# Kernel tuning notes

Hardware: AMD Instinct MI355X
Metric: run time of the kernel (lower is better)

## Reference

```python
import jax, jax.numpy as jnp
import numpy as np

HIDDEN = 1024
BATCH = 32
SRC_LEN = 2048
NEG_BIG = -1e10


def setup_inputs() -> dict:
    key = jax.random.key(0)
    k1, k2, k3, k4, k5, k6 = jax.random.split(key, 6)
    s = 1.0 / np.sqrt(2 * HIDDEN)
    return {
        "decoder_hidden": jax.random.normal(k1, (BATCH, HIDDEN), dtype=jnp.float32),
        "encoder_outputs": jax.random.normal(k2, (BATCH, SRC_LEN, HIDDEN), dtype=jnp.float32),
        "mask": jax.random.randint(k3, (BATCH, SRC_LEN), 0, 2, dtype=jnp.int32),
        # attn: Linear(2H -> H). Store as (2H, H) so x @ W matches torch x @ W.T
        "attn_W": jax.random.uniform(k4, (2 * HIDDEN, HIDDEN), jnp.float32, -s, s),
        "attn_b": jax.random.uniform(k5, (HIDDEN,), jnp.float32, -s, s),
        # v: Linear(H -> 1, bias=False), stored as (H,)
        "v_w": jax.random.uniform(k6, (HIDDEN,), jnp.float32, -1.0 / np.sqrt(HIDDEN), 1.0 / np.sqrt(HIDDEN)),
    }


def reference(decoder_hidden, encoder_outputs, mask, attn_W, attn_b, v_w):
    # Split the concat-linear: [dec, enc] @ W == dec @ W_dec + enc @ W_enc (same math, no big concat)
    W_dec, W_enc = attn_W[:HIDDEN], attn_W[HIDDEN:]
    dec_proj = decoder_hidden @ W_dec + attn_b            # (B, H)
    enc_proj = jnp.einsum("bsh,hk->bsk", encoder_outputs, W_enc)  # (B, S, H)
    energy = jnp.tanh(dec_proj[:, None, :] + enc_proj)    # (B, S, H)
    attention = jnp.einsum("bsh,h->bs", energy, v_w)      # (B, S)
    attention = jnp.where(mask == 0, NEG_BIG, attention)
    attention_weights = jax.nn.softmax(attention, axis=1)  # (B, S)
    context = jnp.einsum("bs,bsh->bh", attention_weights, encoder_outputs)  # (B, H)
    return attention_weights, context
```

## Files before the change

### kernel.cpp

```cpp
#include <hip/hip_runtime.h>
#include <hip/hip_bf16.h>
#include <math.h>

#define HIDDEN 1024
#define BATCH 32
#define SRC_LEN 2048
#define NROWS (BATCH * SRC_LEN)
#define NEG_BIG -10000000000.0f

typedef __attribute__((ext_vector_type(8))) short bf16x8;
typedef __attribute__((ext_vector_type(4))) float f32x4;
typedef __attribute__((ext_vector_type(4))) unsigned uint32x4;

static __device__ __forceinline__ unsigned short f2bf(float f) {
  unsigned u = __float_as_uint(f);
  u = u + 0x7fffu + ((u >> 16) & 1u);
  return (unsigned short)(u >> 16);
}
static __device__ __forceinline__ unsigned pack2(float a, float b) {
  return (unsigned)f2bf(a) | ((unsigned)f2bf(b) << 16);
}

__global__ __launch_bounds__(256) void k_wt(
    const float* __restrict__ W, unsigned short* __restrict__ WT) {
  __shared__ float ts[64][65];
  const int hy = blockIdx.y * 64, nx = blockIdx.x * 64;
  const int tid = threadIdx.x;
#pragma unroll
  for (int i = 0; i < 16; ++i) {
    int idx = tid + i * 256, r = idx >> 6, c = idx & 63;
    ts[r][c] = W[(HIDDEN + hy + r) * HIDDEN + nx + c];
  }
  __syncthreads();
#pragma unroll
  for (int i = 0; i < 16; ++i) {
    int idx = tid + i * 256, rn = idx >> 6, ch = idx & 63;
    WT[(nx + rn) * HIDDEN + hy + ch] = f2bf(ts[ch][rn]);
  }
}

__global__ __launch_bounds__(256) void k_dec_part(
    const float* __restrict__ dh, const float* __restrict__ W,
    float* __restrict__ decpart) {
  const int kl = threadIdx.x & 63;
  const int bq = threadIdx.x >> 6;
  const int k = blockIdx.x * 64 + kl;
  const int h0 = blockIdx.y * 64;
  __shared__ float dh_s[64][33];
#pragma unroll
  for (int i = 0; i < 8; ++i) {
    int idx = threadIdx.x + i * 256;
    int b = idx >> 6, hh = idx & 63;
    dh_s[hh][b] = dh[b * HIDDEN + h0 + hh];
  }
  __syncthreads();
  float acc[8] = {0.f, 0.f, 0.f, 0.f, 0.f, 0.f, 0.f, 0.f};
#pragma unroll
  for (int hh = 0; hh < 64; ++hh) {
    float w = W[(h0 + hh) * HIDDEN + k];
#pragma unroll
    for (int bb = 0; bb < 8; ++bb) acc[bb] += dh_s[hh][bq * 8 + bb] * w;
  }
#pragma unroll
  for (int bb = 0; bb < 8; ++bb)
    decpart[blockIdx.y * (BATCH * HIDDEN) + (bq * 8 + bb) * HIDDEN + k] = acc[bb];
}

__global__ __launch_bounds__(256) void k_dec_reduce(
    const float* __restrict__ decpart, const float* __restrict__ bias,
    float* __restrict__ out) {
  int e = blockIdx.x * 256 + threadIdx.x;
  float s = bias[e & (HIDDEN - 1)];
#pragma unroll
  for (int hc = 0; hc < 16; ++hc) s += decpart[hc * (BATCH * HIDDEN) + e];
  out[e] = s;
}

#define BM 128
#define BN 256
#define BK 64
#define NT (HIDDEN / BK)

__global__ __launch_bounds__(512, 2) void k_energy_mfma(
    const float* __restrict__ enc, const unsigned short* __restrict__ WT,
    const float* __restrict__ dec_proj, const float* __restrict__ v_w,
    float* __restrict__ part) {
  __shared__ unsigned short As[2][BM * BK];
  __shared__ unsigned short Bs[2][BN * BK];
  __shared__ float red[4][BM];

  const int tid = threadIdx.x;
  const int lane = tid & 63;
  const int wid = tid >> 6;
  const int wm = wid >> 2;
  const int wn = wid & 3;
  const int l16 = lane & 15;
  const int kg = lane >> 4;

  const int bid = blockIdx.x;
  const int l = (bid & 7) * 256 + (bid >> 3);
  const int n0 = (l & 3) * BN;
  const int row0 = (l >> 2) * BM;
  const int b = row0 >> 11;

  f32x4 acc[4][4];
#pragma unroll
  for (int m = 0; m < 4; ++m)
#pragma unroll
    for (int n = 0; n < 4; ++n) acc[m][n] = (f32x4){0.f, 0.f, 0.f, 0.f};

  const float4* enc4 = (const float4*)enc;
  const uint32x4* WT4 = (const uint32x4*)WT;

  float4 pa[4];
  uint32x4 pb[4];

#define LOADAB(t)                                                         \
  do {                                                                    \
    int h0 = (t) * BK;                                                    \
    _Pragma("unroll") for (int i = 0; i < 4; ++i) {                       \
      int chunk = tid + i * 512;                                          \
      int r = chunk >> 4, c4 = chunk & 15;                                \
      pa[i] = enc4[(size_t)(row0 + r) * 256 + (h0 >> 2) + c4];            \
    }                                                                     \
    _Pragma("unroll") for (int i = 0; i < 4; ++i) {                       \
      int chunk = tid + i * 512;                                          \
      int nr = chunk >> 3, c16 = chunk & 7;                               \
      pb[i] = WT4[(size_t)(n0 + nr) * 128 + (h0 >> 3) + c16];             \
    }                                                                     \
  } while (0)

#define STOREAB(bufi)                                                     \
  do {                                                                    \
    _Pragma("unroll") for (int i = 0; i < 4; ++i) {                       \
      int chunk = tid + i * 512;                                          \
      int r = chunk >> 4, c4 = chunk & 15;                                \
      unsigned off = r * 128 + ((c4 * 8) ^ ((r & 7) << 4));               \
      uint2 u;                                                            \
      u.x = pack2(pa[i].x, pa[i].y);                                      \
      u.y = pack2(pa[i].z, pa[i].w);                                      \
      *(uint2*)((char*)As[bufi] + off) = u;                               \
    }                                                                     \
    _Pragma("unroll") for (int i = 0; i < 4; ++i) {                       \
      int chunk = tid + i * 512;                                          \
      int nr = chunk >> 3, c16 = chunk & 7;                               \
      unsigned off = nr * 128 + ((c16 * 16) ^ ((nr & 7) << 4));           \
      *(uint32x4*)((char*)Bs[bufi] + off) = pb[i];                        \
    }                                                                     \
  } while (0)

  LOADAB(0);
  STOREAB(0);
  __syncthreads();

  for (int t = 0; t < NT; ++t) {
    const int cur = t & 1;
    if (t + 1 < NT) LOADAB(t + 1);

    __builtin_amdgcn_s_setprio(1);
#pragma unroll
    for (int ks = 0; ks < 2; ++ks) {
      bf16x8 af[4], bv[4];
#pragma unroll
      for (int m = 0; m < 4; ++m) {
        int r = wm * 64 + m * 16 + l16;
        unsigned off = r * 128 + ((ks * 64 + kg * 16) ^ ((r & 7) << 4));
        af[m] = *(const bf16x8*)((const char*)As[cur] + off);
      }
#pragma unroll
      for (int n = 0; n < 4; ++n) {
        int c = wn * 64 + n * 16 + l16;
        unsigned off = c * 128 + ((ks * 64 + kg * 16) ^ ((c & 7) << 4));
        bv[n] = *(const bf16x8*)((const char*)Bs[cur] + off);
      }
#pragma unroll
      for (int m = 0; m < 4; ++m)
#pragma unroll
        for (int n = 0; n < 4; ++n)
          acc[m][n] = __builtin_amdgcn_mfma_f32_16x16x32_bf16(
              af[m], bv[n], acc[m][n], 0, 0, 0);
    }
    __builtin_amdgcn_s_setprio(0);

    if (t + 1 < NT) STOREAB(cur ^ 1);
    __syncthreads();
  }

  float dv[4], vv[4];
#pragma unroll
  for (int n = 0; n < 4; ++n) {
    int kc = n0 + wn * 64 + n * 16 + l16;
    dv[n] = dec_proj[b * HIDDEN + kc];
    vv[n] = v_w[kc];
  }
#pragma unroll
  for (int m = 0; m < 4; ++m) {
#pragma unroll
    for (int r = 0; r < 4; ++r) {
      float p = 0.f;
#pragma unroll
      for (int n = 0; n < 4; ++n) {
        float x = dv[n] + acc[m][n][r];
        float t = 1.f - 2.f / (__expf(2.f * x) + 1.f);
        p += t * vv[n];
      }
      p += __shfl_xor(p, 1);
      p += __shfl_xor(p, 2);
      p += __shfl_xor(p, 4);
      p += __shfl_xor(p, 8);
      if (l16 == 0) red[wn][wm * 64 + m * 16 + kg * 4 + r] = p;
    }
  }
  __syncthreads();
  if (tid < BM) {
    float s = red[0][tid] + red[1][tid] + red[2][tid] + red[3][tid];
    part[(size_t)(l & 3) * NROWS + row0 + tid] = s;
  }
#undef LOADAB
#undef STOREAB
}

__global__ __launch_bounds__(256) void k_softmax(
    const float* __restrict__ part, const int* __restrict__ mask,
    float* __restrict__ out_w) {
  int b = blockIdx.x, tid = threadIdx.x;
  __shared__ float red[4], red2[4];
  float l[8];
  float m = -INFINITY;
#pragma unroll
  for (int j = 0; j < 8; ++j) {
    int s = tid + 256 * j;
    int row = b * SRC_LEN + s;
    float x = part[row] + part[NROWS + row] + part[2 * NROWS + row] +
              part[3 * NROWS + row];
    l[j] = (mask[row] == 0) ? NEG_BIG : x;
    m = fmaxf(m, l[j]);
  }
#pragma unroll
  for (int off = 32; off; off >>= 1) m = fmaxf(m, __shfl_xor(m, off));
  if ((tid & 63) == 0) red[tid >> 6] = m;
  __syncthreads();
  m = fmaxf(fmaxf(red[0], red[1]), fmaxf(red[2], red[3]));
  float sum = 0.f;
#pragma unroll
  for (int j = 0; j < 8; ++j) {
    l[j] = expf(l[j] - m);
    sum += l[j];
  }
#pragma unroll
  for (int off = 32; off; off >>= 1) sum += __shfl_xor(sum, off);
  if ((tid & 63) == 0) red2[tid >> 6] = sum;
  __syncthreads();
  sum = red2[0] + red2[1] + red2[2] + red2[3];
  float inv = 1.f / sum;
#pragma unroll
  for (int j = 0; j < 8; ++j) out_w[b * SRC_LEN + tid + 256 * j] = l[j] * inv;
}

__global__ __launch_bounds__(256) void k_ctx_partial(
    const float* __restrict__ w, const float* __restrict__ enc,
    float* __restrict__ part) {
  int b = blockIdx.x, sg = blockIdx.y, tid = threadIdx.x;
  const float4* enc4 = (const float4*)enc;
  float4 acc = {0.f, 0.f, 0.f, 0.f};
  int s0 = sg * 128;
#pragma unroll 4
  for (int s = 0; s < 128; ++s) {
    float ws = w[b * SRC_LEN + s0 + s];
    float4 e = enc4[(size_t)(b * SRC_LEN + s0 + s) * 256 + tid];
    acc.x += ws * e.x;
    acc.y += ws * e.y;
    acc.z += ws * e.z;
    acc.w += ws * e.w;
  }
  ((float4*)part)[(b * 16 + sg) * 256 + tid] = acc;
}

__global__ __launch_bounds__(256) void k_ctx_reduce(
    const float* __restrict__ part, float* __restrict__ ctx) {
  int b = blockIdx.x, tid = threadIdx.x;
  float4 acc = {0.f, 0.f, 0.f, 0.f};
#pragma unroll
  for (int sg = 0; sg < 16; ++sg) {
    float4 p = ((const float4*)part)[(b * 16 + sg) * 256 + tid];
    acc.x += p.x;
    acc.y += p.y;
    acc.z += p.z;
    acc.w += p.w;
  }
  ((float4*)ctx)[b * 256 + tid] = acc;
}

extern "C" void kernel_launch(void* const* d_in, const int* in_sizes, int n_in,
                              void* d_out, int out_size, void* d_ws, size_t ws_size,
                              hipStream_t stream) {
  const float* dh = (const float*)d_in[0];
  const float* enc = (const float*)d_in[1];
  const int* mask = (const int*)d_in[2];
  const float* attn_W = (const float*)d_in[3];
  const float* attn_b = (const float*)d_in[4];
  const float* v_w = (const float*)d_in[5];

  float* out_w = (float*)d_out;
  float* out_ctx = (float*)d_out + NROWS;

  float* ws = (float*)d_ws;
  float* part = ws;
  float* dec_proj = ws + 4 * NROWS;
  float* ctxpart = dec_proj + BATCH * HIDDEN;
  float* decpart = ctxpart + BATCH * 16 * HIDDEN;
  unsigned short* WT = (unsigned short*)(decpart + 16 * BATCH * HIDDEN);

  k_wt<<<dim3(16, 16), 256, 0, stream>>>(attn_W, WT);
  k_dec_part<<<dim3(16, 16), 256, 0, stream>>>(dh, attn_W, decpart);
  k_dec_reduce<<<dim3(128), 256, 0, stream>>>(decpart, attn_b, dec_proj);
  k_energy_mfma<<<dim3(2048), 512, 0, stream>>>(enc, WT, dec_proj, v_w, part);
  k_softmax<<<dim3(BATCH), 256, 0, stream>>>(part, mask, out_w);
  k_ctx_partial<<<dim3(BATCH, 16), 256, 0, stream>>>(out_w, enc, ctxpart);
  k_ctx_reduce<<<dim3(BATCH), 256, 0, stream>>>(ctxpart, out_ctx);
}
```

Before: 272.3 us.

## Triple-buffer LDS with two register prefetch stages and lighter barriers

```diff
diff --git a/kernel.cpp b/kernel.cpp
--- a/kernel.cpp
+++ b/kernel.cpp
@@ -85,8 +85,8 @@
     const float* __restrict__ enc, const unsigned short* __restrict__ WT,
     const float* __restrict__ dec_proj, const float* __restrict__ v_w,
     float* __restrict__ part) {
-  __shared__ unsigned short As[2][BM * BK];
-  __shared__ unsigned short Bs[2][BN * BK];
+  __shared__ unsigned short As[3][BM * BK];
+  __shared__ unsigned short Bs[3][BN * BK];
   __shared__ float red[4][BM];
 
   const int tid = threadIdx.x;
@@ -112,10 +112,10 @@
   const float4* enc4 = (const float4*)enc;
   const uint32x4* WT4 = (const uint32x4*)WT;
 
-  float4 pa[4];
-  uint32x4 pb[4];
-
-#define LOADAB(t)                                                         \
+  float4 pa0[4], pa1[4];
+  uint32x4 pb0[4], pb1[4];
+
+#define LOADAB(t, pa, pb)                                                 \
   do {                                                                    \
     int h0 = (t) * BK;                                                    \
     _Pragma("unroll") for (int i = 0; i < 4; ++i) {                       \
@@ -130,7 +130,7 @@
     }                                                                     \
   } while (0)
 
-#define STOREAB(bufi)                                                     \
+#define STOREAB(bufi, pa, pb)                                             \
   do {                                                                    \
     _Pragma("unroll") for (int i = 0; i < 4; ++i) {                       \
       int chunk = tid + i * 512;                                          \
@@ -149,41 +149,56 @@
     }                                                                     \
   } while (0)
 
-  LOADAB(0);
-  STOREAB(0);
-  __syncthreads();
-
-  for (int t = 0; t < NT; ++t) {
-    const int cur = t & 1;
-    if (t + 1 < NT) LOADAB(t + 1);
-
-    __builtin_amdgcn_s_setprio(1);
-#pragma unroll
-    for (int ks = 0; ks < 2; ++ks) {
-      bf16x8 af[4], bv[4];
-#pragma unroll
-      for (int m = 0; m < 4; ++m) {
-        int r = wm * 64 + m * 16 + l16;
-        unsigned off = r * 128 + ((ks * 64 + kg * 16) ^ ((r & 7) << 4));
-        af[m] = *(const bf16x8*)((const char*)As[cur] + off);
-      }
-#pragma unroll
-      for (int n = 0; n < 4; ++n) {
-        int c = wn * 64 + n * 16 + l16;
-        unsigned off = c * 128 + ((ks * 64 + kg * 16) ^ ((c & 7) << 4));
-        bv[n] = *(const bf16x8*)((const char*)Bs[cur] + off);
-      }
-#pragma unroll
-      for (int m = 0; m < 4; ++m)
-#pragma unroll
-        for (int n = 0; n < 4; ++n)
-          acc[m][n] = __builtin_amdgcn_mfma_f32_16x16x32_bf16(
-              af[m], bv[n], acc[m][n], 0, 0, 0);
-    }
-    __builtin_amdgcn_s_setprio(0);
-
-    if (t + 1 < NT) STOREAB(cur ^ 1);
-    __syncthreads();
+#define MFMA_STEP(bufi)                                                   \
+  do {                                                                    \
+    __builtin_amdgcn_s_setprio(1);                                        \
+    _Pragma("unroll") for (int ks = 0; ks < 2; ++ks) {                    \
+      bf16x8 af[4], bv[4];                                                \
+      _Pragma("unroll") for (int m = 0; m < 4; ++m) {                     \
+        int r = wm * 64 + m * 16 + l16;                                   \
+        unsigned off = r * 128 + ((ks * 64 + kg * 16) ^ ((r & 7) << 4));  \
+        af[m] = *(const bf16x8*)((const char*)As[bufi] + off);            \
+      }                                                                   \
+      _Pragma("unroll") for (int n = 0; n < 4; ++n) {                     \
+        int c = wn * 64 + n * 16 + l16;                                   \
+        unsigned off = c * 128 + ((ks * 64 + kg * 16) ^ ((c & 7) << 4));  \
+        bv[n] = *(const bf16x8*)((const char*)Bs[bufi] + off);            \
+      }                                                                   \
+      _Pragma("unroll") for (int m = 0; m < 4; ++m)                       \
+          _Pragma("unroll") for (int n = 0; n < 4; ++n)                   \
+              acc[m][n] = __builtin_amdgcn_mfma_f32_16x16x32_bf16(        \
+                  af[m], bv[n], acc[m][n], 0, 0, 0);                      \
+    }                                                                     \
+    __builtin_amdgcn_s_setprio(0);                                        \
+  } while (0)
+
+#define SOFT_BARRIER()                                  \
+  do {                                                  \
+    asm volatile("s_waitcnt lgkmcnt(0)" ::: "memory");  \
+    __builtin_amdgcn_s_barrier();                       \
+  } while (0)
+
+  LOADAB(0, pa0, pb0);
+  LOADAB(1, pa1, pb1);
+  STOREAB(0, pa0, pb0);
+  SOFT_BARRIER();
+
+  int q0 = 0;
+  for (int t = 0; t < NT; t += 2) {
+    int q1 = q0 + 1; if (q1 == 3) q1 = 0;
+    int q2 = q1 + 1; if (q2 == 3) q2 = 0;
+
+    if (t + 2 < NT) LOADAB(t + 2, pa0, pb0);
+    MFMA_STEP(q0);
+    if (t + 1 < NT) STOREAB(q1, pa1, pb1);
+    SOFT_BARRIER();
+
+    if (t + 3 < NT) LOADAB(t + 3, pa1, pb1);
+    MFMA_STEP(q1);
+    if (t + 2 < NT) STOREAB(q2, pa0, pb0);
+    SOFT_BARRIER();
+
+    q0 = q2;
   }
 
   float dv[4], vv[4];
@@ -218,6 +233,8 @@
   }
 #undef LOADAB
 #undef STOREAB
+#undef MFMA_STEP
+#undef SOFT_BARRIER
 }
 
 __global__ __launch_bounds__(256) void k_softmax(
```

Result: slower. 288.7 us (+6.0%).
